# Performance work log

Measured on AMD Instinct MI355X. Metric: run time of the kernel, lower is better.

Reference implementation:

```python
import jax, jax.numpy as jnp
import numpy as np

N = 131072
E = 524288
H = 128
EPS = 1e-5

def _layernorm(h, g, b):
    mu = jnp.mean(h, axis=-1, keepdims=True)
    var = jnp.mean((h - mu) ** 2, axis=-1, keepdims=True)
    return (h - mu) * jax.lax.rsqrt(var + EPS) * g + b

def _node_to_node(x, senders, receivers, valid, num_nodes, params):
    # two-way (symmetrized) message passing: gather + scatter_add, then MLP+LN
    W1, b1, W2, b2, W3, b3, g, beta = params
    tws = jnp.concatenate([senders, receivers])
    twr = jnp.concatenate([receivers, senders])
    msg = x[tws]  # [2E', H] gather
    if valid is not None:
        msg = jnp.where(jnp.concatenate([valid, valid])[:, None], msg, 0.0)
    agg = jax.ops.segment_sum(msg, twr, num_segments=num_nodes)  # scatter_add
    h = jax.nn.gelu(agg @ W1 + b1, approximate=False)
    h = jax.nn.gelu(h @ W2 + b2, approximate=False)
    h = h @ W3 + b3
    return _layernorm(h, g, beta)

def setup_inputs() -> dict:
    key = jax.random.key(0)
    ks = jax.random.split(key, 20)
    s = 0.05
    inp = {
        "x": jax.random.normal(ks[0], (N, H), dtype=jnp.float32),
        "edge_index": jax.random.randint(ks[1], (2, E), 0, N, dtype=jnp.int32),
        "pool_p": jax.random.normal(ks[2], (H,), dtype=jnp.float32),
    }
    names = ["dW1", "db1", "dW2", "db2", "dW3", "db3", "dg", "dbeta",
             "uW1", "ub1", "uW2", "ub2", "uW3", "ub3", "ug", "ubeta"]
    shapes = [(H, H), (H,), (H, H), (H,), (H, H), (H,), (H,), (H,),
              (2 * H, H), (H,), (H, H), (H,), (H, H), (H,), (H,), (H,)]
    for i, (nm, sh) in enumerate(zip(names, shapes)):
        if nm in ("dg", "ug"):
            inp[nm] = jnp.ones(sh, dtype=jnp.float32)
        elif nm in ("dbeta", "ubeta") or nm.startswith(("db", "ub")):
            inp[nm] = jnp.zeros(sh, dtype=jnp.float32)
        else:
            inp[nm] = jax.random.normal(ks[3 + i], sh, dtype=jnp.float32) * s
    return inp

def reference(x, edge_index, pool_p,
              dW1, db1, dW2, db2, dW3, db3, dg, dbeta,
              uW1, ub1, uW2, ub2, uW3, ub3, ug, ubeta):
    senders, receivers = edge_index[0], edge_index[1]
    k = N // 2  # TopKPooling ratio=0.5

    # ---- down: TopKPooling ----
    score = x @ pool_p / jnp.linalg.norm(pool_p)  # [N]
    _, perm = jax.lax.top_k(score, k)             # kept node indices
    x_skip = x
    x_p = x[perm] * jnp.tanh(score[perm])[:, None]  # [k, H]
    mask = jnp.zeros((N,), dtype=bool).at[perm].set(True)
    mapping = jnp.zeros((N,), dtype=jnp.int32).at[perm].set(
        jnp.arange(k, dtype=jnp.int32))
    valid = mask[senders] & mask[receivers]
    ps, pr = mapping[senders], mapping[receivers]

    # down conv on pooled graph
    x_d = _node_to_node(x_p, ps, pr, valid, k,
                        (dW1, db1, dW2, db2, dW3, db3, dg, dbeta))

    # ---- up: unpool (indexed scatter write) + skip concat + up conv ----
    recovered = jnp.zeros_like(x_skip).at[perm].set(x_d)
    x_u = jnp.concatenate([recovered, x_skip], axis=-1)  # [N, 2H]
    out = _node_to_node(x_u, senders, receivers, None, N,
                        (uW1, ub1, uW2, ub2, uW3, ub3, ug, ubeta))
    return out
```

## Files before the change

### kernel.cpp

```cpp
#include <hip/hip_runtime.h>

#define N_NODES 131072
#define N_EDGES 524288
#define K_TOP   65536
#define LN_EPS  1e-5f
#define N_TILES (N_NODES / 64)

typedef unsigned int u32;
typedef unsigned short u16;
typedef unsigned long long u64;

typedef __attribute__((ext_vector_type(8))) short bf8;
typedef __attribute__((ext_vector_type(4))) float f4;

#define ST_OFF    0
#define CANON_OFF (64u<<10)
#define PART_OFF  (576u<<10)
#define KEYS_OFF  (1u<<20)
#define TVAL_OFF  (2u<<20)
#define KEPT_OFF  ((2u<<20)+(512u<<10))
#define SBUF_OFF  (3u<<20)
#define DEG_OFF   (34u<<20)
#define OFF_OFF   (35u<<20)
#define ADJ_OFF   (36u<<20)


#define C_DW1 0
#define C_DB1 16384
#define C_DW2 16512
#define C_DB2 32896
#define C_DW3 33024
#define C_DB3 49408
#define C_DG  49536
#define C_DBE 49664
#define C_UW1 49792
#define C_UB1 82560
#define C_UW2 82688
#define C_UB2 99072
#define C_UW3 99200
#define C_UB3 115584
#define C_UG  115712
#define C_UBE 115840
#define C_TOT 115968
#define CT_DW1 115968
#define CT_DW2 132352
#define CT_DW3 148736
#define CT_UW1 165120
#define CT_UW2 197888
#define CT_UW3 214272
#define CT_TOT 230656

__device__ __forceinline__ float bflo(u32 u){ return __uint_as_float(u << 16); }
__device__ __forceinline__ float bfhi(u32 u){ return __uint_as_float(u & 0xFFFF0000u); }
__device__ __forceinline__ float bf2f(u16 v){ return __uint_as_float(((u32)v) << 16); }
__device__ __forceinline__ u32 f2bf(float f){
  u32 u = __float_as_uint(f);
  return (u + 0x7FFFu + ((u >> 16) & 1u)) >> 16;
}
__device__ __forceinline__ float gelu_f(float x){
  return 0.5f * x * (1.0f + erff(x * 0.7071067811865476f));
}
__device__ __forceinline__ float2 f2add(float2 a, float2 b){
  return make_float2(a.x + b.x, a.y + b.y);
}

__device__ __forceinline__ int swz16(int row, int cc){
  return row * 128 + ((cc ^ (row & 15)) * 8);
}

__device__ __forceinline__ bf8 ld_bf16_chunk(const u32* __restrict__ rowp, int s, int quad){
  uint4 v = *(const uint4*)(rowp + s * 16 + quad * 4);
  return __builtin_bit_cast(bf8, v);
}
__device__ __forceinline__ bf8 scale_bf16_chunk(const u32* __restrict__ rowp, int s, int quad, float tv){
  uint4 v = *(const uint4*)(rowp + s * 16 + quad * 4);
  uint4 q;
  q.x = f2bf(bflo(v.x) * tv) | (f2bf(bfhi(v.x) * tv) << 16);
  q.y = f2bf(bflo(v.y) * tv) | (f2bf(bfhi(v.y) * tv) << 16);
  q.z = f2bf(bflo(v.z) * tv) | (f2bf(bfhi(v.z) * tv) << 16);
  q.w = f2bf(bflo(v.w) * tv) | (f2bf(bfhi(v.w) * tv) << 16);
  return __builtin_bit_cast(bf8, q);
}
__device__ __forceinline__ bf8 cvt_f32_chunk(const float* __restrict__ rowp, int s, int quad, float tv){
  const float* p = rowp + s * 32 + quad * 8;
  float4 f0 = *(const float4*)p;
  float4 f1 = *(const float4*)(p + 4);
  uint4 q;
  q.x = f2bf(f0.x * tv) | (f2bf(f0.y * tv) << 16);
  q.y = f2bf(f0.z * tv) | (f2bf(f0.w * tv) << 16);
  q.z = f2bf(f1.x * tv) | (f2bf(f1.y * tv) << 16);
  q.w = f2bf(f1.z * tv) | (f2bf(f1.w * tv) << 16);
  return __builtin_bit_cast(bf8, q);
}

__device__ __forceinline__ void gemm_ab(const u16* ws, const bf8 a[4], int mn, int quad, f4 acc[8]){
  #pragma unroll
  for (int s = 0; s < 4; s++){
    #pragma unroll
    for (int j = 0; j < 8; j++){
      bf8 b = *(const bf8*)&ws[swz16(j * 16 + mn, s * 4 + quad)];
      acc[j] = __builtin_amdgcn_mfma_f32_16x16x32_bf16(a[s], b, acc[j], 0, 0, 0);
    }
  }
}

struct SelState {
  u64 prefix;
  u32 krem, eqcnt;
  int is_f32;
  u32 pad;
  double inv_norm;
  u32 eqlist[4096];
  u64 eqkey[4096];
};

struct P16 { const void* q[16]; };

__global__ void k_detect(const u32* __restrict__ xw, SelState* st){
  int t = threadIdx.x;
  int cnt = 0;
  for (int i = t; i < 4096; i += 256){
    u32 w = xw[(size_t)i * 2048];
    u32 e = (w >> 23) & 0xFFu;
    if (e >= 97u && e <= 135u) cnt++;
  }
  __shared__ int sh[256];
  sh[t] = cnt; __syncthreads();
  for (int o = 128; o > 0; o >>= 1){ if (t < o) sh[t] += sh[t+o]; __syncthreads(); }
  if (t == 0){
    st->is_f32 = (sh[0] >= 3072) ? 1 : 0;
    st->prefix = 0; st->krem = K_TOP; st->eqcnt = 0;
  }
}

__global__ void k_canon(P16 ps, const SelState* __restrict__ st, u16* __restrict__ canon){
  int i = blockIdx.x * 256 + threadIdx.x;
  if (i >= CT_TOT) return;
  int isf = st->is_f32;
  if (i < C_TOT){
    const int off[17] = {C_DW1,C_DB1,C_DW2,C_DB2,C_DW3,C_DB3,C_DG,C_DBE,
                         C_UW1,C_UB1,C_UW2,C_UB2,C_UW3,C_UB3,C_UG,C_UBE,C_TOT};
    int seg = 0;
    #pragma unroll
    for (int s2 = 0; s2 < 16; s2++) if (i >= off[s2+1]) seg = s2 + 1;
    int j = i - off[seg];
    if (isf) canon[i] = (u16)f2bf(((const float*)ps.q[seg])[j]);
    else     canon[i] = ((const u16*)ps.q[seg])[j];
  } else {
    const int dst[7] = {CT_DW1, CT_DW2, CT_DW3, CT_UW1, CT_UW2, CT_UW3, CT_TOT};
    const int wq[6]  = {0, 2, 4, 8, 10, 12};
    int g = i;
    int seg = 0;
    #pragma unroll
    for (int s2 = 0; s2 < 6; s2++) if (g >= dst[s2+1]) seg = s2 + 1;
    int loc = g - dst[seg];
    int K = (seg == 3) ? 256 : 128;
    int n = loc / K, k = loc % K;
    int src = k * 128 + n;
    if (isf) canon[g] = (u16)f2bf(((const float*)ps.q[wq[seg]])[src]);
    else     canon[g] = ((const u16*)ps.q[wq[seg]])[src];
  }
}

__global__ __launch_bounds__(256) void k_score(const void* __restrict__ xraw, const void* __restrict__ praw,
                        const SelState* __restrict__ st,
                        u64* __restrict__ keys, float* __restrict__ tval){
  int t = threadIdx.x, lane = t & 63, w = t >> 6;
  int n = blockIdx.x * 4 + w;
  double d, ps;
  if (st->is_f32){
    const float* xf = (const float*)xraw + (size_t)n * 128;
    const float* pf = (const float*)praw;
    double p0 = (double)pf[lane], p1 = (double)pf[64 + lane];
    d  = (double)xf[lane] * p0 + (double)xf[64 + lane] * p1;
    ps = p0 * p0 + p1 * p1;
  } else {
    const u32* xw = (const u32*)xraw + (size_t)n * 64;
    const u32* pw = (const u32*)praw;
    u32 xx = xw[lane], pv = pw[lane];
    double p0 = (double)bflo(pv), p1 = (double)bfhi(pv);
    d  = (double)bflo(xx) * p0 + (double)bfhi(xx) * p1;
    ps = p0 * p0 + p1 * p1;
  }
  for (int o = 32; o > 0; o >>= 1){
    d  += __shfl_down(d,  o, 64);
    ps += __shfl_down(ps, o, 64);
  }
  if (lane == 0){
    double sc = d * (1.0 / sqrt(ps));
    u64 u = (u64)__double_as_longlong(sc);
    u64 key = (u & 0x8000000000000000ULL) ? ~u : (u | 0x8000000000000000ULL);
    keys[n] = key;
    tval[n] = tanhf((float)sc);
  }
}

__global__ __launch_bounds__(256) void k_histp(const u64* __restrict__ keys,
                                               const SelState* __restrict__ st,
                                               u32* __restrict__ partial, int pass){
  __shared__ u32 h[256];
  int t = threadIdx.x;
  h[t] = 0;
  __syncthreads();
  u64 pref = st->prefix;
  int sh_d = 56 - 8 * pass;
  for (int n = blockIdx.x * 256 + t; n < N_NODES; n += 256 * 256){
    u64 k = keys[n];
    bool m = (pass == 0) ? true : ((k >> (sh_d + 8)) == pref);
    if (m) atomicAdd(&h[(u32)((k >> sh_d) & 255)], 1u);
  }
  __syncthreads();
  partial[blockIdx.x * 256 + t] = h[t];
}

__global__ void k_scanp(const u32* __restrict__ partial, SelState* st){
  __shared__ u32 tot[256];
  int t = threadIdx.x;
  u32 s = 0;
  for (int b = 0; b < 256; b++) s += partial[b * 256 + t];
  tot[t] = s;
  __syncthreads();
  if (t == 0){
    u32 target = st->krem;
    u32 cum = 0; int chosen = 255;
    for (int b = 255; b >= 0; b--){
      if (cum + tot[b] >= target){ chosen = b; break; }
      cum += tot[b];
    }
    st->prefix = (st->prefix << 8) | (u64)(u32)chosen;
    st->krem = target - cum;
  }
}

__global__ void k_mark(const u64* __restrict__ keys, SelState* st, u32* __restrict__ kept,
                       u32* __restrict__ deg){
  int n = blockIdx.x * blockDim.x + threadIdx.x;
  u64 k = keys[n];
  u32 t32 = (u32)(k >> 32);
  u32 T = (u32)st->prefix;
  kept[n] = (t32 > T) ? 1u : 0u;
  deg[n] = 0u;
  if (t32 == T){
    u32 i = atomicAdd(&st->eqcnt, 1u);
    if (i < 4096){ st->eqlist[i] = (u32)n; st->eqkey[i] = k; }
  }
}

__global__ void k_tie(SelState* st, u32* __restrict__ kept){
  u32 m = st->eqcnt; if (m > 4096) m = 4096;
  u32 r = st->krem;
  for (u32 i = threadIdx.x; i < m; i += blockDim.x){
    u64 ki = st->eqkey[i]; u32 ii = st->eqlist[i];
    u32 rank = 0;
    for (u32 j = 0; j < m; j++){
      u64 kj = st->eqkey[j];
      rank += (kj > ki || (kj == ki && st->eqlist[j] < ii)) ? 1u : 0u;
    }
    if (rank < r) kept[ii] = 1u;
  }
}

__global__ __launch_bounds__(256) void k_deg(const int* __restrict__ se, const int* __restrict__ re,
                                             u32* __restrict__ deg){
  int e = blockIdx.x * 256 + threadIdx.x;
  int s = se[e], r = re[e];
  atomicAdd(&deg[s], 1u);
  atomicAdd(&deg[r], 1u);
}

__global__ __launch_bounds__(256) void k_scan1(const u32* __restrict__ deg, u32* __restrict__ bsum){
  __shared__ u32 sh[256];
  int t = threadIdx.x;
  int base = blockIdx.x * 1024 + t * 4;
  u32 s = deg[base] + deg[base+1] + deg[base+2] + deg[base+3];
  sh[t] = s; __syncthreads();
  for (int o = 128; o > 0; o >>= 1){ if (t < o) sh[t] += sh[t+o]; __syncthreads(); }
  if (t == 0) bsum[blockIdx.x] = sh[0];
}

__global__ void k_scan2(u32* __restrict__ bsum){
  __shared__ u32 sh[128];
  int t = threadIdx.x;
  u32 v = bsum[t];
  sh[t] = v; __syncthreads();
  for (int o = 1; o < 128; o <<= 1){
    u32 x = (t >= o) ? sh[t-o] : 0u;
    __syncthreads();
    sh[t] += x;
    __syncthreads();
  }
  bsum[t] = sh[t] - v;
}

__global__ __launch_bounds__(256) void k_scan3(const u32* __restrict__ bsum,
                                               const u32* __restrict__ deg, u32* __restrict__ off,
                                               u32* __restrict__ gcur, u32* __restrict__ zrow){
  __shared__ u32 sh[256];
  int t = threadIdx.x;
  int base = blockIdx.x * 1024 + t * 4;
  u32 v0 = deg[base], v1 = deg[base+1], v2 = deg[base+2], v3 = deg[base+3];
  u32 s = v0 + v1 + v2 + v3;
  sh[t] = s; __syncthreads();
  for (int o = 1; o < 256; o <<= 1){
    u32 x = (t >= o) ? sh[t-o] : 0u;
    __syncthreads();
    sh[t] += x;
    __syncthreads();
  }
  u32 ex = sh[t] - s + bsum[blockIdx.x];
  if ((t & 127) == 0) gcur[base >> 9] = ex;
  off[base]   = ex; ex += v0;
  off[base+1] = ex; ex += v1;
  off[base+2] = ex; ex += v2;
  off[base+3] = ex;
  if (blockIdx.x == 0){
    if (t == 0) off[N_NODES] = 2u * N_EDGES;
    if (t < 64) zrow[t] = 0u;
  }
}

__global__ __launch_bounds__(256) void k_bin(const int* __restrict__ se, const int* __restrict__ re,
                                             u32* __restrict__ gcur, u32* __restrict__ pairs){
  __shared__ u32 cnt[256], sc[256], base[256], cur[256], gpos[256];
  __shared__ u32 stage[8192];
  int t = threadIdx.x;
  cnt[t] = 0;
  __syncthreads();
  int e0 = blockIdx.x * 4096;
  for (int i = t; i < 4096; i += 256){
    int s = se[e0 + i], r = re[e0 + i];
    atomicAdd(&cnt[(u32)r >> 9], 1u);
    atomicAdd(&cnt[(u32)s >> 9], 1u);
  }
  __syncthreads();
  sc[t] = cnt[t];
  __syncthreads();
  for (int o = 1; o < 256; o <<= 1){
    u32 x = (t >= o) ? sc[t - o] : 0u;
    __syncthreads();
    sc[t] += x;
    __syncthreads();
  }
  base[t] = sc[t] - cnt[t];
  cur[t] = base[t];
  gpos[t] = atomicAdd(&gcur[t], cnt[t]);
  __syncthreads();
  for (int i = t; i < 4096; i += 256){
    u32 s = (u32)se[e0 + i], r = (u32)re[e0 + i];
    u32 b1 = r >> 9, p1 = ((r & 511u) << 17) | s;
    u32 b2 = s >> 9, p2 = ((s & 511u) << 17) | r;
    stage[atomicAdd(&cur[b1], 1u)] = p1;
    stage[atomicAdd(&cur[b2], 1u)] = p2;
  }
  __syncthreads();
  int lane = t & 63, wv = t >> 6;
  for (int b = wv; b < 256; b += 4){
    u32 n = cnt[b], src = base[b], dst = gpos[b];
    for (u32 i = lane; i < n; i += 64)
      pairs[dst + i] = stage[src + i];
  }
}

__global__ __launch_bounds__(256) void k_place(const u32* __restrict__ off,
                                               const u32* __restrict__ pairs,
                                               u32* __restrict__ adj){
  __shared__ u32 offl[513];
  __shared__ u32 curl[512];
  int b = blockIdx.x, t = threadIdx.x;
  for (int i = t; i < 513; i += 256) offl[i] = off[b * 512 + i];
  for (int i = t; i < 512; i += 256) curl[i] = 0;
  __syncthreads();
  u32 beg = offl[0], end = offl[512];
  for (u32 i = beg + t; i < end; i += 256){
    u32 p = pairs[i];
    u32 nl = p >> 17, m = p & 0x1FFFFu;
    u32 slot = offl[nl] + atomicAdd(&curl[nl], 1u);
    adj[slot] = m;
  }
}


__global__ __launch_bounds__(256, 3) void k_proj_down(
    const void* __restrict__ xraw, const float* __restrict__ tval,
    const u16* __restrict__ W1T, const SelState* __restrict__ st,
    const u32* __restrict__ kept, u32* __restrict__ S)
{
  __shared__ u16 w1s[128 * 128];
  __shared__ u16 os[64 * 128];
  int t = threadIdx.x, lane = t & 63, wv = t >> 6;
  int m0 = wv * 16, mn = lane & 15, quad = lane >> 4;

  for (int i = t; i < 2048; i += 256){
    int row = i >> 4, cc = i & 15;
    *(uint4*)&w1s[swz16(row, cc)] = *(const uint4*)(W1T + row * 128 + cc * 8);
  }
  int isf = st->is_f32;
  __syncthreads();

  for (int tile = blockIdx.x; tile < N_TILES; tile += gridDim.x){
    int row0 = tile * 64;
    int arow = row0 + m0 + mn;
    float tv = tval[arow];
    bf8 a[4];
    if (isf){
      const float* xf = (const float*)xraw + (size_t)arow * 128;
      #pragma unroll
      for (int s = 0; s < 4; s++) a[s] = cvt_f32_chunk(xf, s, quad, tv);
    } else {
      const u32* xw = (const u32*)xraw + (size_t)arow * 64;
      #pragma unroll
      for (int s = 0; s < 4; s++) a[s] = scale_bf16_chunk(xw, s, quad, tv);
    }
    f4 acc[8];
    #pragma unroll
    for (int j = 0; j < 8; j++){ acc[j][0]=0.f; acc[j][1]=0.f; acc[j][2]=0.f; acc[j][3]=0.f; }
    gemm_ab(w1s, a, mn, quad, acc);

    #pragma unroll
    for (int j = 0; j < 8; j++){
      int c = j * 16 + mn;
      #pragma unroll
      for (int rg = 0; rg < 4; rg++){
        int row = m0 + quad * 4 + rg;
        os[row * 128 + ((c >> 3) ^ (row & 15)) * 8 + (c & 7)] = (u16)f2bf(acc[j][rg]);
      }
    }
    __builtin_amdgcn_wave_barrier();
    int rl = m0 + (lane >> 2), qt = lane & 3;
    u32 kp = kept[row0 + rl];
    u32* out = S + (size_t)(row0 + rl) * 64;
    #pragma unroll
    for (int i = 0; i < 4; i++){
      int cc = qt * 4 + i;
      uint4 w = *(const uint4*)&os[swz16(rl, cc)];
      if (!kp){ w.x = 0; w.y = 0; w.z = 0; w.w = 0; }
      *(uint4*)(out + cc * 4) = w;
    }
    __builtin_amdgcn_wave_barrier();
  }
}

__global__ __launch_bounds__(256, 2) void k_proj_up(
    const u32* __restrict__ R, const void* __restrict__ xraw,
    const u16* __restrict__ W1T, const SelState* __restrict__ st,
    u32* __restrict__ S2)
{
  __shared__ u16 was[128 * 128];
  __shared__ u16 wbs[128 * 128];
  __shared__ u16 os[64 * 128];
  int t = threadIdx.x, lane = t & 63, wv = t >> 6;
  int m0 = wv * 16, mn = lane & 15, quad = lane >> 4;

  for (int i = t; i < 2048; i += 256){
    int row = i >> 4, cc = i & 15;
    *(uint4*)&was[swz16(row, cc)] = *(const uint4*)(W1T + row * 256 + cc * 8);
    *(uint4*)&wbs[swz16(row, cc)] = *(const uint4*)(W1T + row * 256 + 128 + cc * 8);
  }
  int isf = st->is_f32;
  __syncthreads();

  for (int tile = blockIdx.x; tile < N_TILES; tile += gridDim.x){
    int row0 = tile * 64;
    int arow = row0 + m0 + mn;
    bf8 a[4];
    const u32* rp = R + (size_t)arow * 64;
    #pragma unroll
    for (int s = 0; s < 4; s++) a[s] = ld_bf16_chunk(rp, s, quad);
    f4 acc[8];
    #pragma unroll
    for (int j = 0; j < 8; j++){ acc[j][0]=0.f; acc[j][1]=0.f; acc[j][2]=0.f; acc[j][3]=0.f; }
    gemm_ab(was, a, mn, quad, acc);

    if (isf){
      const float* xf = (const float*)xraw + (size_t)arow * 128;
      #pragma unroll
      for (int s = 0; s < 4; s++) a[s] = cvt_f32_chunk(xf, s, quad, 1.0f);
    } else {
      const u32* xw = (const u32*)xraw + (size_t)arow * 64;
      #pragma unroll
      for (int s = 0; s < 4; s++) a[s] = ld_bf16_chunk(xw, s, quad);
    }
    gemm_ab(wbs, a, mn, quad, acc);

    #pragma unroll
    for (int j = 0; j < 8; j++){
      int c = j * 16 + mn;
      #pragma unroll
      for (int rg = 0; rg < 4; rg++){
        int row = m0 + quad * 4 + rg;
        os[row * 128 + ((c >> 3) ^ (row & 15)) * 8 + (c & 7)] = (u16)f2bf(acc[j][rg]);
      }
    }
    __builtin_amdgcn_wave_barrier();
    int rl = m0 + (lane >> 2), qt = lane & 3;
    u32* out = S2 + (size_t)(row0 + rl) * 64;
    #pragma unroll
    for (int i = 0; i < 4; i++){
      int cc = qt * 4 + i;
      *(uint4*)(out + cc * 4) = *(const uint4*)&os[swz16(rl, cc)];
    }
    __builtin_amdgcn_wave_barrier();
  }
}

template<int IS_DOWN>
__device__ __forceinline__ const u32* rowsel(const u32* __restrict__ Smsg, u32 e,
                                             const u32* __restrict__ kept,
                                             const u32* __restrict__ zrow){
  const u32* p = Smsg + (size_t)e * 64;
  if (IS_DOWN) p = kept[e] ? p : zrow;
  return p;
}

template<int IS_DOWN>
__global__ __launch_bounds__(256, 4) void k_agg(
    const u32* __restrict__ Smsg, const u32* __restrict__ off, const u32* __restrict__ adj,
    const u16* __restrict__ cb1, const u32* __restrict__ kept,
    const u32* __restrict__ zrow, u32* __restrict__ H)
{
  int t = threadIdx.x, lane = t & 63, wv = t >> 6;
  float b1l = bf2f(cb1[2 * lane]), b1h = bf2f(cb1[2 * lane + 1]);
  int base = blockIdx.x * 16 + wv * 4;
  #pragma unroll 1
  for (int rr = 0; rr < 4; rr++){
    int n = base + rr;
    if (IS_DOWN && !kept[n]){ H[(size_t)n * 64 + lane] = 0u; continue; }
    u32 jb = off[n], je = off[n + 1];
    float2 a = make_float2(0.f, 0.f);
    u32 j = jb;
    for (; j + 8 <= je; j += 8){
      const u32* r0 = rowsel<IS_DOWN>(Smsg, adj[j],   kept, zrow);
      const u32* r1 = rowsel<IS_DOWN>(Smsg, adj[j+1], kept, zrow);
      const u32* r2 = rowsel<IS_DOWN>(Smsg, adj[j+2], kept, zrow);
      const u32* r3 = rowsel<IS_DOWN>(Smsg, adj[j+3], kept, zrow);
      const u32* r4 = rowsel<IS_DOWN>(Smsg, adj[j+4], kept, zrow);
      const u32* r5 = rowsel<IS_DOWN>(Smsg, adj[j+5], kept, zrow);
      const u32* r6 = rowsel<IS_DOWN>(Smsg, adj[j+6], kept, zrow);
      const u32* r7 = rowsel<IS_DOWN>(Smsg, adj[j+7], kept, zrow);
      u32 w0 = r0[lane], w1 = r1[lane], w2 = r2[lane], w3 = r3[lane];
      u32 w4 = r4[lane], w5 = r5[lane], w6 = r6[lane], w7 = r7[lane];
      float2 v0 = make_float2(bflo(w0), bfhi(w0));
      float2 v1 = make_float2(bflo(w1), bfhi(w1));
      float2 v2 = make_float2(bflo(w2), bfhi(w2));
      float2 v3 = make_float2(bflo(w3), bfhi(w3));
      float2 v4 = make_float2(bflo(w4), bfhi(w4));
      float2 v5 = make_float2(bflo(w5), bfhi(w5));
      float2 v6 = make_float2(bflo(w6), bfhi(w6));
      float2 v7 = make_float2(bflo(w7), bfhi(w7));
      a = f2add(a, f2add(f2add(f2add(v0, v1), f2add(v2, v3)),
                         f2add(f2add(v4, v5), f2add(v6, v7))));
    }
    for (; j + 4 <= je; j += 4){
      const u32* r0 = rowsel<IS_DOWN>(Smsg, adj[j],   kept, zrow);
      const u32* r1 = rowsel<IS_DOWN>(Smsg, adj[j+1], kept, zrow);
      const u32* r2 = rowsel<IS_DOWN>(Smsg, adj[j+2], kept, zrow);
      const u32* r3 = rowsel<IS_DOWN>(Smsg, adj[j+3], kept, zrow);
      u32 w0 = r0[lane], w1 = r1[lane], w2 = r2[lane], w3 = r3[lane];
      float2 v0 = make_float2(bflo(w0), bfhi(w0));
      float2 v1 = make_float2(bflo(w1), bfhi(w1));
      float2 v2 = make_float2(bflo(w2), bfhi(w2));
      float2 v3 = make_float2(bflo(w3), bfhi(w3));
      a = f2add(a, f2add(f2add(v0, v1), f2add(v2, v3)));
    }
    for (; j < je; j++){
      const u32* r0 = rowsel<IS_DOWN>(Smsg, adj[j], kept, zrow);
      u32 w = r0[lane];
      a = f2add(a, make_float2(bflo(w), bfhi(w)));
    }
    H[(size_t)n * 64 + lane] = f2bf(gelu_f(a.x + b1l)) | (f2bf(gelu_f(a.y + b1h)) << 16);
  }
}

template<int IS_DOWN>
__global__ __launch_bounds__(256, 2) void k_mlp(
    const u32* __restrict__ H,
    const u16* __restrict__ cW2T, const u16* __restrict__ cb2,
    const u16* __restrict__ cW3T, const u16* __restrict__ cb3,
    const u16* __restrict__ cg, const u16* __restrict__ cbe,
    const u32* __restrict__ kept, const SelState* __restrict__ st,
    u32* __restrict__ Rout, void* __restrict__ fout)
{
  __shared__ u16 w2s[128 * 128];
  __shared__ u16 w3s[128 * 128];
  __shared__ u16 os[64 * 128];
  int t = threadIdx.x, lane = t & 63, wv = t >> 6;
  int m0 = wv * 16, mn = lane & 15, quad = lane >> 4;

  for (int i = t; i < 2048; i += 256){
    int row = i >> 4, cc = i & 15;
    *(uint4*)&w2s[swz16(row, cc)] = *(const uint4*)(cW2T + row * 128 + cc * 8);
    *(uint4*)&w3s[swz16(row, cc)] = *(const uint4*)(cW3T + row * 128 + cc * 8);
  }
  float b2v[8], b3v[8], gv[8], bev[8];
  #pragma unroll
  for (int j = 0; j < 8; j++){
    int c = j * 16 + mn;
    b2v[j] = bf2f(cb2[c]); b3v[j] = bf2f(cb3[c]);
    gv[j]  = bf2f(cg[c]);  bev[j] = bf2f(cbe[c]);
  }
  int isf = st->is_f32;
  __syncthreads();

  for (int tile = blockIdx.x; tile < N_TILES; tile += gridDim.x){
    int row0 = tile * 64;
    int arow = row0 + m0 + mn;

    bf8 a[4];
    const u32* hp = H + (size_t)arow * 64;
    #pragma unroll
    for (int s = 0; s < 4; s++) a[s] = ld_bf16_chunk(hp, s, quad);
    f4 acc[8];
    #pragma unroll
    for (int j = 0; j < 8; j++){ acc[j][0]=0.f; acc[j][1]=0.f; acc[j][2]=0.f; acc[j][3]=0.f; }
    gemm_ab(w2s, a, mn, quad, acc);

    #pragma unroll
    for (int j = 0; j < 8; j++){
      int c = j * 16 + mn;
      #pragma unroll
      for (int rg = 0; rg < 4; rg++){
        int row = m0 + quad * 4 + rg;
        os[row * 128 + ((c >> 3) ^ (row & 15)) * 8 + (c & 7)] = (u16)f2bf(gelu_f(acc[j][rg] + b2v[j]));
      }
    }
    __builtin_amdgcn_wave_barrier();

    #pragma unroll
    for (int s = 0; s < 4; s++) a[s] = *(const bf8*)&os[swz16(m0 + mn, s * 4 + quad)];
    #pragma unroll
    for (int j = 0; j < 8; j++){ acc[j][0]=0.f; acc[j][1]=0.f; acc[j][2]=0.f; acc[j][3]=0.f; }
    gemm_ab(w3s, a, mn, quad, acc);

    #pragma unroll
    for (int j = 0; j < 8; j++){
      #pragma unroll
      for (int rg = 0; rg < 4; rg++) acc[j][rg] += b3v[j];
    }
    float s1[4] = {0.f,0.f,0.f,0.f}, s2[4] = {0.f,0.f,0.f,0.f};
    #pragma unroll
    for (int j = 0; j < 8; j++){
      #pragma unroll
      for (int rg = 0; rg < 4; rg++){
        float v = acc[j][rg];
        s1[rg] += v; s2[rg] += v * v;
      }
    }
    #pragma unroll
    for (int o = 1; o < 16; o <<= 1){
      #pragma unroll
      for (int rg = 0; rg < 4; rg++){
        s1[rg] += __shfl_xor(s1[rg], o, 64);
        s2[rg] += __shfl_xor(s2[rg], o, 64);
      }
    }
    float mu[4], rs[4];
    #pragma unroll
    for (int rg = 0; rg < 4; rg++){
      mu[rg] = s1[rg] * 0.0078125f;
      float var = s2[rg] * 0.0078125f - mu[rg] * mu[rg];
      rs[rg] = rsqrtf(var + LN_EPS);
    }
    #pragma unroll
    for (int j = 0; j < 8; j++){
      #pragma unroll
      for (int rg = 0; rg < 4; rg++)
        acc[j][rg] = (acc[j][rg] - mu[rg]) * rs[rg] * gv[j] + bev[j];
    }

    if (!IS_DOWN && isf){
      float* fo = (float*)fout;
      #pragma unroll
      for (int j = 0; j < 8; j++){
        #pragma unroll
        for (int rg = 0; rg < 4; rg++)
          fo[(size_t)(row0 + m0 + quad * 4 + rg) * 128 + j * 16 + mn] = acc[j][rg];
      }
      continue;
    }

    __builtin_amdgcn_wave_barrier();
    #pragma unroll
    for (int j = 0; j < 8; j++){
      int c = j * 16 + mn;
      #pragma unroll
      for (int rg = 0; rg < 4; rg++){
        int row = m0 + quad * 4 + rg;
        os[row * 128 + ((c >> 3) ^ (row & 15)) * 8 + (c & 7)] = (u16)f2bf(acc[j][rg]);
      }
    }
    __builtin_amdgcn_wave_barrier();
    int rl = m0 + (lane >> 2), qt = lane & 3;
    u32 kp = IS_DOWN ? kept[row0 + rl] : 1u;
    u32* out = (IS_DOWN ? Rout : (u32*)fout) + (size_t)(row0 + rl) * 64;
    #pragma unroll
    for (int i = 0; i < 4; i++){
      int cc = qt * 4 + i;
      uint4 w = *(const uint4*)&os[swz16(rl, cc)];
      if (!kp){ w.x = 0; w.y = 0; w.z = 0; w.w = 0; }
      *(uint4*)(out + cc * 4) = w;
    }
    __builtin_amdgcn_wave_barrier();
  }
}


extern "C" void kernel_launch(void* const* d_in, const int* in_sizes, int n_in,
                              void* d_out, int out_size, void* d_ws, size_t ws_size,
                              hipStream_t stream)
{
  const void* x     = d_in[0];
  const int* eidx   = (const int*)d_in[1];
  const void* poolp = d_in[2];
  const int* senders = eidx;
  const int* receivers = eidx + N_EDGES;

  char* ws = (char*)d_ws;
  SelState* st = (SelState*)(ws + ST_OFF);
  u16*  canon  = (u16*) (ws + CANON_OFF);
  u32*  partial= (u32*) (ws + PART_OFF);
  u64*  keys   = (u64*) (ws + KEYS_OFF);
  float* tval  = (float*)(ws + TVAL_OFF);
  u32*  kept   = (u32*) (ws + KEPT_OFF);
  u32*  Sbuf   = (u32*) (ws + SBUF_OFF);
  u32*  deg    = (u32*) (ws + DEG_OFF);
  u32*  off    = (u32*) (ws + OFF_OFF);
  u32*  adj    = (u32*) (ws + ADJ_OFF);
  u32*  bsum   = partial;
  u32*  gcur   = partial + 512;
  u32*  zrow   = partial + 2048;
  u32*  pairs  = Sbuf;
  u32*  Dbuf   = (u32*) d_out;

  P16 ps;
  for (int i = 0; i < 16; i++) ps.q[i] = d_in[3 + i];

  k_detect<<<1, 256, 0, stream>>>((const u32*)x, st);
  k_canon<<<(CT_TOT + 255) / 256, 256, 0, stream>>>(ps, st, canon);
  k_score<<<N_NODES / 4, 256, 0, stream>>>(x, poolp, st, keys, tval);
  for (int pass = 0; pass < 4; pass++){
    k_histp<<<256, 256, 0, stream>>>(keys, st, partial, pass);
    k_scanp<<<1, 256, 0, stream>>>(partial, st);
  }
  k_mark<<<N_NODES / 256, 256, 0, stream>>>(keys, st, kept, deg);
  k_tie<<<1, 256, 0, stream>>>(st, kept);

  k_deg<<<N_EDGES / 256, 256, 0, stream>>>(senders, receivers, deg);
  k_scan1<<<128, 256, 0, stream>>>(deg, bsum);
  k_scan2<<<1, 128, 0, stream>>>(bsum);
  k_scan3<<<128, 256, 0, stream>>>(bsum, deg, off, gcur, zrow);
  k_bin<<<N_EDGES / 4096, 256, 0, stream>>>(senders, receivers, gcur, pairs);
  k_place<<<256, 256, 0, stream>>>(off, pairs, adj);

  k_proj_down<<<768, 256, 0, stream>>>(x, tval, canon + CT_DW1, st, kept, Sbuf);
  k_agg<1><<<N_NODES / 16, 256, 0, stream>>>(Sbuf, off, adj, canon + C_DB1, kept, zrow, Dbuf);
  k_mlp<1><<<512, 256, 0, stream>>>(Dbuf,
      canon + CT_DW2, canon + C_DB2, canon + CT_DW3, canon + C_DB3,
      canon + C_DG, canon + C_DBE, kept, st, Sbuf, nullptr);

  k_proj_up<<<512, 256, 0, stream>>>(Sbuf, x, canon + CT_UW1, st, Dbuf);
  k_agg<0><<<N_NODES / 16, 256, 0, stream>>>(Dbuf, off, adj, canon + C_UB1, kept, zrow, Sbuf);
  k_mlp<0><<<512, 256, 0, stream>>>(Sbuf,
      canon + CT_UW2, canon + C_UB2, canon + CT_UW3, canon + C_UB3,
      canon + C_UG, canon + C_UBE, kept, st, nullptr, d_out);
}
```

Measured before the change: 528.6 us.

## Replace degree scan with fixed-capacity buckets and fold top-k prefix scan into histograms

```diff
diff --git a/kernel.cpp b/kernel.cpp
--- a/kernel.cpp
+++ b/kernel.cpp
@@ -5,6 +5,7 @@
 #define K_TOP   65536
 #define LN_EPS  1e-5f
 #define N_TILES (N_NODES / 64)
+#define BCAP    5120u
 
 typedef unsigned int u32;
 typedef unsigned short u16;
@@ -20,9 +21,7 @@
 #define TVAL_OFF  (2u<<20)
 #define KEPT_OFF  ((2u<<20)+(512u<<10))
 #define SBUF_OFF  (3u<<20)
-#define DEG_OFF   (34u<<20)
-#define OFF_OFF   (35u<<20)
-#define ADJ_OFF   (36u<<20)
+#define ADJ_OFF   (35u<<20)
 
 
 #define C_DW1 0
@@ -116,6 +115,25 @@
 
 struct P16 { const void* q[16]; };
 
+__device__ __forceinline__ void chain_step(const u32* __restrict__ tots, int q,
+                                           u32* sfx, u32* selb, int t,
+                                           u64& pref, u32& target){
+  sfx[t] = tots[q * 256 + t];
+  __syncthreads();
+  for (int o = 1; o < 256; o <<= 1){
+    u32 x = (t + o < 256) ? sfx[t + o] : 0u;
+    __syncthreads();
+    sfx[t] += x;
+    __syncthreads();
+  }
+  u32 above = (t == 255) ? 0u : sfx[t + 1];
+  if (sfx[t] >= target && above < target){ selb[0] = (u32)t; selb[1] = target - above; }
+  __syncthreads();
+  pref = (pref << 8) | (u64)selb[0];
+  target = selb[1];
+  __syncthreads();
+}
+
 __global__ void k_detect(const u32* __restrict__ xw, SelState* st){
   int t = threadIdx.x;
   int cnt = 0;
@@ -133,8 +151,11 @@
   }
 }
 
-__global__ void k_canon(P16 ps, const SelState* __restrict__ st, u16* __restrict__ canon){
+__global__ void k_canon(P16 ps, const SelState* __restrict__ st, u16* __restrict__ canon,
+                        u32* __restrict__ tots, u32* __restrict__ gcur){
   int i = blockIdx.x * 256 + threadIdx.x;
+  if (i < 1024) tots[i] = 0u;
+  if (i < 256)  gcur[i] = (u32)i * BCAP;
   if (i >= CT_TOT) return;
   int isf = st->is_f32;
   if (i < C_TOT){
@@ -196,13 +217,17 @@
 }
 
 __global__ __launch_bounds__(256) void k_histp(const u64* __restrict__ keys,
-                                               const SelState* __restrict__ st,
-                                               u32* __restrict__ partial, int pass){
+                                               u32* __restrict__ tots, int pass){
+  __shared__ u32 sfx[256];
+  __shared__ u32 selb[2];
   __shared__ u32 h[256];
   int t = threadIdx.x;
+  u64 pref = 0;
+  u32 target = K_TOP;
+  for (int q = 0; q < pass; q++)
+    chain_step(tots, q, sfx, selb, t, pref, target);
   h[t] = 0;
   __syncthreads();
-  u64 pref = st->prefix;
   int sh_d = 56 - 8 * pass;
   for (int n = blockIdx.x * 256 + t; n < N_NODES; n += 256 * 256){
     u64 k = keys[n];
@@ -210,46 +235,42 @@
     if (m) atomicAdd(&h[(u32)((k >> sh_d) & 255)], 1u);
   }
   __syncthreads();
-  partial[blockIdx.x * 256 + t] = h[t];
-}
-
-__global__ void k_scanp(const u32* __restrict__ partial, SelState* st){
-  __shared__ u32 tot[256];
+  if (h[t]) atomicAdd(&tots[pass * 256 + t], h[t]);
+}
+
+__global__ __launch_bounds__(256) void k_mark(const u64* __restrict__ keys,
+                                              const u32* __restrict__ tots,
+                                              SelState* st, u32* __restrict__ kept){
+  __shared__ u32 sfx[256];
+  __shared__ u32 selb[2];
   int t = threadIdx.x;
-  u32 s = 0;
-  for (int b = 0; b < 256; b++) s += partial[b * 256 + t];
-  tot[t] = s;
-  __syncthreads();
-  if (t == 0){
-    u32 target = st->krem;
-    u32 cum = 0; int chosen = 255;
-    for (int b = 255; b >= 0; b--){
-      if (cum + tot[b] >= target){ chosen = b; break; }
-      cum += tot[b];
-    }
-    st->prefix = (st->prefix << 8) | (u64)(u32)chosen;
-    st->krem = target - cum;
-  }
-}
-
-__global__ void k_mark(const u64* __restrict__ keys, SelState* st, u32* __restrict__ kept,
-                       u32* __restrict__ deg){
-  int n = blockIdx.x * blockDim.x + threadIdx.x;
+  u64 pref = 0;
+  u32 target = K_TOP;
+  for (int q = 0; q < 4; q++)
+    chain_step(tots, q, sfx, selb, t, pref, target);
+  u32 T = (u32)pref;
+  int n = blockIdx.x * 256 + t;
   u64 k = keys[n];
   u32 t32 = (u32)(k >> 32);
-  u32 T = (u32)st->prefix;
   kept[n] = (t32 > T) ? 1u : 0u;
-  deg[n] = 0u;
   if (t32 == T){
     u32 i = atomicAdd(&st->eqcnt, 1u);
     if (i < 4096){ st->eqlist[i] = (u32)n; st->eqkey[i] = k; }
   }
 }
 
-__global__ void k_tie(SelState* st, u32* __restrict__ kept){
+__global__ __launch_bounds__(256) void k_tie(const u32* __restrict__ tots,
+                                             SelState* st, u32* __restrict__ kept){
+  __shared__ u32 sfx[256];
+  __shared__ u32 selb[2];
+  int t = threadIdx.x;
+  u64 pref = 0;
+  u32 target = K_TOP;
+  for (int q = 0; q < 4; q++)
+    chain_step(tots, q, sfx, selb, t, pref, target);
+  u32 r = target;
   u32 m = st->eqcnt; if (m > 4096) m = 4096;
-  u32 r = st->krem;
-  for (u32 i = threadIdx.x; i < m; i += blockDim.x){
+  for (u32 i = t; i < m; i += 256){
     u64 ki = st->eqkey[i]; u32 ii = st->eqlist[i];
     u32 rank = 0;
     for (u32 j = 0; j < m; j++){
@@ -257,65 +278,6 @@
       rank += (kj > ki || (kj == ki && st->eqlist[j] < ii)) ? 1u : 0u;
     }
     if (rank < r) kept[ii] = 1u;
-  }
-}
-
-__global__ __launch_bounds__(256) void k_deg(const int* __restrict__ se, const int* __restrict__ re,
-                                             u32* __restrict__ deg){
-  int e = blockIdx.x * 256 + threadIdx.x;
-  int s = se[e], r = re[e];
-  atomicAdd(&deg[s], 1u);
-  atomicAdd(&deg[r], 1u);
-}
-
-__global__ __launch_bounds__(256) void k_scan1(const u32* __restrict__ deg, u32* __restrict__ bsum){
-  __shared__ u32 sh[256];
-  int t = threadIdx.x;
-  int base = blockIdx.x * 1024 + t * 4;
-  u32 s = deg[base] + deg[base+1] + deg[base+2] + deg[base+3];
-  sh[t] = s; __syncthreads();
-  for (int o = 128; o > 0; o >>= 1){ if (t < o) sh[t] += sh[t+o]; __syncthreads(); }
-  if (t == 0) bsum[blockIdx.x] = sh[0];
-}
-
-__global__ void k_scan2(u32* __restrict__ bsum){
-  __shared__ u32 sh[128];
-  int t = threadIdx.x;
-  u32 v = bsum[t];
-  sh[t] = v; __syncthreads();
-  for (int o = 1; o < 128; o <<= 1){
-    u32 x = (t >= o) ? sh[t-o] : 0u;
-    __syncthreads();
-    sh[t] += x;
-    __syncthreads();
-  }
-  bsum[t] = sh[t] - v;
-}
-
-__global__ __launch_bounds__(256) void k_scan3(const u32* __restrict__ bsum,
-                                               const u32* __restrict__ deg, u32* __restrict__ off,
-                                               u32* __restrict__ gcur, u32* __restrict__ zrow){
-  __shared__ u32 sh[256];
-  int t = threadIdx.x;
-  int base = blockIdx.x * 1024 + t * 4;
-  u32 v0 = deg[base], v1 = deg[base+1], v2 = deg[base+2], v3 = deg[base+3];
-  u32 s = v0 + v1 + v2 + v3;
-  sh[t] = s; __syncthreads();
-  for (int o = 1; o < 256; o <<= 1){
-    u32 x = (t >= o) ? sh[t-o] : 0u;
-    __syncthreads();
-    sh[t] += x;
-    __syncthreads();
-  }
-  u32 ex = sh[t] - s + bsum[blockIdx.x];
-  if ((t & 127) == 0) gcur[base >> 9] = ex;
-  off[base]   = ex; ex += v0;
-  off[base+1] = ex; ex += v1;
-  off[base+2] = ex; ex += v2;
-  off[base+3] = ex;
-  if (blockIdx.x == 0){
-    if (t == 0) off[N_NODES] = 2u * N_EDGES;
-    if (t < 64) zrow[t] = 0u;
   }
 }
 
@@ -361,21 +323,39 @@
   }
 }
 
-__global__ __launch_bounds__(256) void k_place(const u32* __restrict__ off,
+__global__ __launch_bounds__(256) void k_place(const u32* __restrict__ gcur,
                                                const u32* __restrict__ pairs,
-                                               u32* __restrict__ adj){
-  __shared__ u32 offl[513];
-  __shared__ u32 curl[512];
+                                               u32* __restrict__ adj,
+                                               u32* __restrict__ off, u32* __restrict__ end){
+  __shared__ u32 cnt[512], cur[512], lo[512], ex2[256];
   int b = blockIdx.x, t = threadIdx.x;
-  for (int i = t; i < 513; i += 256) offl[i] = off[b * 512 + i];
-  for (int i = t; i < 512; i += 256) curl[i] = 0;
-  __syncthreads();
-  u32 beg = offl[0], end = offl[512];
-  for (u32 i = beg + t; i < end; i += 256){
-    u32 p = pairs[i];
-    u32 nl = p >> 17, m = p & 0x1FFFFu;
-    u32 slot = offl[nl] + atomicAdd(&curl[nl], 1u);
-    adj[slot] = m;
+  u32 base = (u32)b * BCAP;
+  u32 total = gcur[b] - base;
+  cnt[t] = 0; cnt[t + 256] = 0; cur[t] = 0; cur[t + 256] = 0;
+  __syncthreads();
+  for (u32 i = t; i < total; i += 256)
+    atomicAdd(&cnt[pairs[base + i] >> 17], 1u);
+  __syncthreads();
+  u32 c0 = cnt[2 * t], c1 = cnt[2 * t + 1];
+  ex2[t] = c0 + c1;
+  __syncthreads();
+  for (int o = 1; o < 256; o <<= 1){
+    u32 x = (t >= o) ? ex2[t - o] : 0u;
+    __syncthreads();
+    ex2[t] += x;
+    __syncthreads();
+  }
+  u32 e0 = ex2[t] - c0 - c1;
+  int n0 = b * 512 + 2 * t;
+  off[n0]     = base + e0;        end[n0]     = base + e0 + c0;
+  off[n0 + 1] = base + e0 + c0;   end[n0 + 1] = base + e0 + c0 + c1;
+  lo[2 * t] = e0; lo[2 * t + 1] = e0 + c0;
+  __syncthreads();
+  for (u32 i = t; i < total; i += 256){
+    u32 p = pairs[base + i];
+    u32 nl = p >> 17;
+    u32 slot = base + lo[nl] + atomicAdd(&cur[nl], 1u);
+    adj[slot] = p & 0x1FFFFu;
   }
 }
 
@@ -504,19 +484,11 @@
 }
 
 template<int IS_DOWN>
-__device__ __forceinline__ const u32* rowsel(const u32* __restrict__ Smsg, u32 e,
-                                             const u32* __restrict__ kept,
-                                             const u32* __restrict__ zrow){
-  const u32* p = Smsg + (size_t)e * 64;
-  if (IS_DOWN) p = kept[e] ? p : zrow;
-  return p;
-}
-
-template<int IS_DOWN>
 __global__ __launch_bounds__(256, 4) void k_agg(
-    const u32* __restrict__ Smsg, const u32* __restrict__ off, const u32* __restrict__ adj,
+    const u32* __restrict__ Smsg, const u32* __restrict__ off, const u32* __restrict__ end,
+    const u32* __restrict__ adj,
     const u16* __restrict__ cb1, const u32* __restrict__ kept,
-    const u32* __restrict__ zrow, u32* __restrict__ H)
+    u32* __restrict__ H)
 {
   int t = threadIdx.x, lane = t & 63, wv = t >> 6;
   float b1l = bf2f(cb1[2 * lane]), b1h = bf2f(cb1[2 * lane + 1]);
@@ -525,20 +497,20 @@
   for (int rr = 0; rr < 4; rr++){
     int n = base + rr;
     if (IS_DOWN && !kept[n]){ H[(size_t)n * 64 + lane] = 0u; continue; }
-    u32 jb = off[n], je = off[n + 1];
+    u32 jb = off[n], je = end[n];
     float2 a = make_float2(0.f, 0.f);
     u32 j = jb;
     for (; j + 8 <= je; j += 8){
-      const u32* r0 = rowsel<IS_DOWN>(Smsg, adj[j],   kept, zrow);
-      const u32* r1 = rowsel<IS_DOWN>(Smsg, adj[j+1], kept, zrow);
-      const u32* r2 = rowsel<IS_DOWN>(Smsg, adj[j+2], kept, zrow);
-      const u32* r3 = rowsel<IS_DOWN>(Smsg, adj[j+3], kept, zrow);
-      const u32* r4 = rowsel<IS_DOWN>(Smsg, adj[j+4], kept, zrow);
-      const u32* r5 = rowsel<IS_DOWN>(Smsg, adj[j+5], kept, zrow);
-      const u32* r6 = rowsel<IS_DOWN>(Smsg, adj[j+6], kept, zrow);
-      const u32* r7 = rowsel<IS_DOWN>(Smsg, adj[j+7], kept, zrow);
-      u32 w0 = r0[lane], w1 = r1[lane], w2 = r2[lane], w3 = r3[lane];
-      u32 w4 = r4[lane], w5 = r5[lane], w6 = r6[lane], w7 = r7[lane];
+      u32 e0 = adj[j],   e1 = adj[j+1], e2 = adj[j+2], e3 = adj[j+3];
+      u32 e4 = adj[j+4], e5 = adj[j+5], e6 = adj[j+6], e7 = adj[j+7];
+      u32 w0 = Smsg[(size_t)e0 * 64 + lane];
+      u32 w1 = Smsg[(size_t)e1 * 64 + lane];
+      u32 w2 = Smsg[(size_t)e2 * 64 + lane];
+      u32 w3 = Smsg[(size_t)e3 * 64 + lane];
+      u32 w4 = Smsg[(size_t)e4 * 64 + lane];
+      u32 w5 = Smsg[(size_t)e5 * 64 + lane];
+      u32 w6 = Smsg[(size_t)e6 * 64 + lane];
+      u32 w7 = Smsg[(size_t)e7 * 64 + lane];
       float2 v0 = make_float2(bflo(w0), bfhi(w0));
       float2 v1 = make_float2(bflo(w1), bfhi(w1));
       float2 v2 = make_float2(bflo(w2), bfhi(w2));
@@ -551,11 +523,11 @@
                          f2add(f2add(v4, v5), f2add(v6, v7))));
     }
     for (; j + 4 <= je; j += 4){
-      const u32* r0 = rowsel<IS_DOWN>(Smsg, adj[j],   kept, zrow);
-      const u32* r1 = rowsel<IS_DOWN>(Smsg, adj[j+1], kept, zrow);
-      const u32* r2 = rowsel<IS_DOWN>(Smsg, adj[j+2], kept, zrow);
-      const u32* r3 = rowsel<IS_DOWN>(Smsg, adj[j+3], kept, zrow);
-      u32 w0 = r0[lane], w1 = r1[lane], w2 = r2[lane], w3 = r3[lane];
+      u32 e0 = adj[j], e1 = adj[j+1], e2 = adj[j+2], e3 = adj[j+3];
+      u32 w0 = Smsg[(size_t)e0 * 64 + lane];
+      u32 w1 = Smsg[(size_t)e1 * 64 + lane];
+      u32 w2 = Smsg[(size_t)e2 * 64 + lane];
+      u32 w3 = Smsg[(size_t)e3 * 64 + lane];
       float2 v0 = make_float2(bflo(w0), bfhi(w0));
       float2 v1 = make_float2(bflo(w1), bfhi(w1));
       float2 v2 = make_float2(bflo(w2), bfhi(w2));
@@ -563,8 +535,7 @@
       a = f2add(a, f2add(f2add(v0, v1), f2add(v2, v3)));
     }
     for (; j < je; j++){
-      const u32* r0 = rowsel<IS_DOWN>(Smsg, adj[j], kept, zrow);
-      u32 w = r0[lane];
+      u32 w = Smsg[(size_t)adj[j] * 64 + lane];
       a = f2add(a, make_float2(bflo(w), bfhi(w)));
     }
     H[(size_t)n * 64 + lane] = f2bf(gelu_f(a.x + b1l)) | (f2bf(gelu_f(a.y + b1h)) << 16);
@@ -717,17 +688,15 @@
   char* ws = (char*)d_ws;
   SelState* st = (SelState*)(ws + ST_OFF);
   u16*  canon  = (u16*) (ws + CANON_OFF);
-  u32*  partial= (u32*) (ws + PART_OFF);
+  u32*  tots   = (u32*) (ws + PART_OFF);
+  u32*  gcur   = (u32*) (ws + PART_OFF + 4096);
   u64*  keys   = (u64*) (ws + KEYS_OFF);
+  u32*  off    = (u32*) (ws + KEYS_OFF);
+  u32*  end    = (u32*) (ws + KEYS_OFF + (512u<<10));
   float* tval  = (float*)(ws + TVAL_OFF);
   u32*  kept   = (u32*) (ws + KEPT_OFF);
   u32*  Sbuf   = (u32*) (ws + SBUF_OFF);
-  u32*  deg    = (u32*) (ws + DEG_OFF);
-  u32*  off    = (u32*) (ws + OFF_OFF);
   u32*  adj    = (u32*) (ws + ADJ_OFF);
-  u32*  bsum   = partial;
-  u32*  gcur   = partial + 512;
-  u32*  zrow   = partial + 2048;
   u32*  pairs  = Sbuf;
   u32*  Dbuf   = (u32*) d_out;
 
@@ -735,30 +704,24 @@
   for (int i = 0; i < 16; i++) ps.q[i] = d_in[3 + i];
 
   k_detect<<<1, 256, 0, stream>>>((const u32*)x, st);
-  k_canon<<<(CT_TOT + 255) / 256, 256, 0, stream>>>(ps, st, canon);
+  k_canon<<<(CT_TOT + 255) / 256, 256, 0, stream>>>(ps, st, canon, tots, gcur);
   k_score<<<N_NODES / 4, 256, 0, stream>>>(x, poolp, st, keys, tval);
-  for (int pass = 0; pass < 4; pass++){
-    k_histp<<<256, 256, 0, stream>>>(keys, st, partial, pass);
-    k_scanp<<<1, 256, 0, stream>>>(partial, st);
-  }
-  k_mark<<<N_NODES / 256, 256, 0, stream>>>(keys, st, kept, deg);
-  k_tie<<<1, 256, 0, stream>>>(st, kept);
-
-  k_deg<<<N_EDGES / 256, 256, 0, stream>>>(senders, receivers, deg);
-  k_scan1<<<128, 256, 0, stream>>>(deg, bsum);
-  k_scan2<<<1, 128, 0, stream>>>(bsum);
-  k_scan3<<<128, 256, 0, stream>>>(bsum, deg, off, gcur, zrow);
+  for (int pass = 0; pass < 4; pass++)
+    k_histp<<<256, 256, 0, stream>>>(keys, tots, pass);
+  k_mark<<<N_NODES / 256, 256, 0, stream>>>(keys, tots, st, kept);
+  k_tie<<<1, 256, 0, stream>>>(tots, st, kept);
+
   k_bin<<<N_EDGES / 4096, 256, 0, stream>>>(senders, receivers, gcur, pairs);
-  k_place<<<256, 256, 0, stream>>>(off, pairs, adj);
+  k_place<<<256, 256, 0, stream>>>(gcur, pairs, adj, off, end);
 
   k_proj_down<<<768, 256, 0, stream>>>(x, tval, canon + CT_DW1, st, kept, Sbuf);
-  k_agg<1><<<N_NODES / 16, 256, 0, stream>>>(Sbuf, off, adj, canon + C_DB1, kept, zrow, Dbuf);
+  k_agg<1><<<N_NODES / 16, 256, 0, stream>>>(Sbuf, off, end, adj, canon + C_DB1, kept, Dbuf);
   k_mlp<1><<<512, 256, 0, stream>>>(Dbuf,
       canon + CT_DW2, canon + C_DB2, canon + CT_DW3, canon + C_DB3,
       canon + C_DG, canon + C_DBE, kept, st, Sbuf, nullptr);
 
   k_proj_up<<<512, 256, 0, stream>>>(Sbuf, x, canon + CT_UW1, st, Dbuf);
-  k_agg<0><<<N_NODES / 16, 256, 0, stream>>>(Dbuf, off, adj, canon + C_UB1, kept, zrow, Sbuf);
+  k_agg<0><<<N_NODES / 16, 256, 0, stream>>>(Dbuf, off, end, adj, canon + C_UB1, kept, Sbuf);
   k_mlp<0><<<512, 256, 0, stream>>>(Sbuf,
       canon + CT_UW2, canon + C_UB2, canon + CT_UW3, canon + C_UB3,
       canon + C_UG, canon + C_UBE, kept, st, nullptr, d_out);
```

After: 449.8 us. 14.9% less time.
